# Kernel tuning notes

Measured on AMD Instinct MI355X. Metric: run time of the kernel, lower is better.

## Reference

```python
import jax, jax.numpy as jnp
import numpy as np

IMAGE_WEIGHT = 0.0736196319
EXAM_WEIGHTS = np.array([0.0736196319, 0.09202453988, 0.1042944785, 0.1042944785,
                         0.1877300613, 0.06257668712, 0.06257668712, 0.2346625767,
                         0.0782208589], dtype=np.float32)


def setup_inputs() -> dict:
    key = jax.random.key(0)
    k1, k2, k3 = jax.random.split(key, 3)
    B, L, C = 128, 8192, 10
    # probabilities / soft labels in (0,1); keep away from exact 0/1 so log() is finite
    pred = jax.random.uniform(k1, (B, L, C), dtype=jnp.float32) * 0.98 + 0.01
    label = jax.random.uniform(k2, (B, L, C), dtype=jnp.float32) * 0.98 + 0.01
    seq_lens = jax.random.randint(k3, (B,), 1, L + 1, dtype=jnp.int32)
    return {"pred": pred, "label": label, "seq_lens": seq_lens}


def reference(pred, label, seq_lens):
    B, L, C = pred.shape
    w = jnp.asarray(EXAM_WEIGHTS, dtype=pred.dtype)          # [9]
    lens = seq_lens.astype(pred.dtype)                        # [B]
    mask = (jnp.arange(L)[None, :] < seq_lens[:, None]).astype(pred.dtype)  # [B, L]

    # ---- exam-level loss: BCE between per-exam masked means, weighted per channel ----
    pm = jnp.einsum('blc,bl->bc', pred[..., 1:], mask) / lens[:, None]   # [B, 9]
    ym = jnp.einsum('blc,bl->bc', label[..., 1:], mask) / lens[:, None]  # [B, 9]
    exam_bce = -(ym * jnp.log(pm) + (1.0 - ym) * jnp.log(1.0 - pm))      # [B, 9]
    exam_loss = jnp.sum(exam_bce * w[None, :])
    total_weights = B * jnp.sum(w)

    # ---- image-level loss: per-element BCE weighted by image_weight * mean(label_0) ----
    p0 = pred[..., 0]   # [B, L]
    y0 = label[..., 0]  # [B, L]
    y0_mean = jnp.sum(y0 * mask, axis=1) / lens                          # [B]
    img_w = IMAGE_WEIGHT * y0_mean                                       # [B]
    img_bce = -(y0 * jnp.log(p0) + (1.0 - y0) * jnp.log(1.0 - p0)) * mask  # [B, L]
    image_loss = jnp.sum(jnp.sum(img_bce, axis=1) * img_w)
    total_weights = total_weights + jnp.sum(img_w * lens)

    return (exam_loss + image_loss) / total_weights
```

## Files before the change

### kernel.cpp

```cpp
#include <hip/hip_runtime.h>


#define L_DIM 8192
#define B_DIM 128
#define C_DIM 10
#define SPLIT 8

#define IMAGE_WEIGHT 0.0736196319f

__device__ __constant__ float EXAM_W[9] = {
    0.0736196319f, 0.09202453988f, 0.1042944785f, 0.1042944785f,
    0.1877300613f, 0.06257668712f, 0.06257668712f, 0.2346625767f,
    0.0782208589f};

__device__ __forceinline__ float bce0(float p, float y) {
  return -(y * __logf(p) + (1.0f - y) * __logf(1.0f - p));
}

__global__ __launch_bounds__(256) void rsna_partial_kernel(
    const float* __restrict__ pred, const float* __restrict__ label,
    const int* __restrict__ seq_lens, float* __restrict__ slots) {
  const int b = blockIdx.x;
  const int s = blockIdx.y;
  const int len = seq_lens[b];
  const int chunk = ((len + 2 * SPLIT - 1) / (2 * SPLIT)) * 2;
  const int start = s * chunk;
  const int end = min(start + chunk, len);

  float sp[9], sl[9];
#pragma unroll
  for (int c = 0; c < 9; ++c) {
    sp[c] = 0.0f;
    sl[c] = 0.0f;
  }
  float sy0 = 0.0f;
  float sbce = 0.0f;

  for (int l = start + 2 * (int)threadIdx.x; l < end; l += 512) {
    const size_t base = ((size_t)b * L_DIM + (size_t)l) * C_DIM;
    if (l + 1 < end) {
      const float4* p4 = reinterpret_cast<const float4*>(pred + base);
      const float4* y4 = reinterpret_cast<const float4*>(label + base);
      float p[20], y[20];
#pragma unroll
      for (int i = 0; i < 5; ++i) {
        float4 pv = p4[i];
        float4 yv = y4[i];
        p[4 * i] = pv.x; p[4 * i + 1] = pv.y; p[4 * i + 2] = pv.z; p[4 * i + 3] = pv.w;
        y[4 * i] = yv.x; y[4 * i + 1] = yv.y; y[4 * i + 2] = yv.z; y[4 * i + 3] = yv.w;
      }
#pragma unroll
      for (int c = 0; c < 9; ++c) {
        sp[c] += p[c + 1] + p[c + 11];
        sl[c] += y[c + 1] + y[c + 11];
      }
      sy0 += y[0] + y[10];
      sbce += bce0(p[0], y[0]) + bce0(p[10], y[10]);
    } else {
      const float2* p2 = reinterpret_cast<const float2*>(pred + base);
      const float2* y2 = reinterpret_cast<const float2*>(label + base);
      float p[10], y[10];
#pragma unroll
      for (int i = 0; i < 5; ++i) {
        float2 pv = p2[i];
        float2 yv = y2[i];
        p[2 * i] = pv.x; p[2 * i + 1] = pv.y;
        y[2 * i] = yv.x; y[2 * i + 1] = yv.y;
      }
#pragma unroll
      for (int c = 0; c < 9; ++c) {
        sp[c] += p[c + 1];
        sl[c] += y[c + 1];
      }
      sy0 += y[0];
      sbce += bce0(p[0], y[0]);
    }
  }

  float vals[20];
#pragma unroll
  for (int c = 0; c < 9; ++c) {
    vals[c] = sp[c];
    vals[9 + c] = sl[c];
  }
  vals[18] = sy0;
  vals[19] = sbce;

#pragma unroll
  for (int i = 0; i < 20; ++i) {
    float v = vals[i];
#pragma unroll
    for (int off = 32; off > 0; off >>= 1) v += __shfl_down(v, off, 64);
    vals[i] = v;
  }

  __shared__ float lds[4][20];
  const int wave = threadIdx.x >> 6;
  const int lane = threadIdx.x & 63;
  if (lane == 0) {
#pragma unroll
    for (int i = 0; i < 20; ++i) lds[wave][i] = vals[i];
  }
  __syncthreads();
  if (threadIdx.x < 20) {
    slots[(b * SPLIT + s) * 20 + (int)threadIdx.x] =
        lds[0][threadIdx.x] + lds[1][threadIdx.x] + lds[2][threadIdx.x] +
        lds[3][threadIdx.x];
  }
}

__global__ __launch_bounds__(128) void rsna_final_kernel(
    const float* __restrict__ slots, const int* __restrict__ seq_lens,
    float* __restrict__ out) {
  const int b = threadIdx.x;
  float r[20];
#pragma unroll
  for (int i = 0; i < 20; ++i) r[i] = 0.0f;
  const float* base = slots + b * SPLIT * 20;
#pragma unroll
  for (int s = 0; s < SPLIT; ++s)
#pragma unroll
    for (int i = 0; i < 20; ++i) r[i] += base[s * 20 + i];

  const float len = (float)seq_lens[b];
  const float inv_len = 1.0f / len;

  float exam = 0.0f;
#pragma unroll
  for (int c = 0; c < 9; ++c) {
    const float pm = r[c] * inv_len;
    const float ym = r[9 + c] * inv_len;
    exam += EXAM_W[c] * (-(ym * __logf(pm) + (1.0f - ym) * __logf(1.0f - pm)));
  }
  const float sy0 = r[18];
  const float sbce = r[19];
  const float img_w = IMAGE_WEIGHT * sy0 * inv_len;
  float numer = exam + sbce * img_w;
  float wext = IMAGE_WEIGHT * sy0;

#pragma unroll
  for (int off = 32; off > 0; off >>= 1) {
    numer += __shfl_down(numer, off, 64);
    wext += __shfl_down(wext, off, 64);
  }

  __shared__ float lds[4];
  if ((threadIdx.x & 63) == 0) {
    const int wave = threadIdx.x >> 6;
    lds[wave * 2] = numer;
    lds[wave * 2 + 1] = wext;
  }
  __syncthreads();
  if (threadIdx.x == 0) {
    float wsum = 0.0f;
#pragma unroll
    for (int c = 0; c < 9; ++c) wsum += EXAM_W[c];
    const float n = lds[0] + lds[2];
    const float w = lds[1] + lds[3];
    out[0] = n / ((float)B_DIM * wsum + w);
  }
}

extern "C" void kernel_launch(void* const* d_in, const int* in_sizes, int n_in,
                              void* d_out, int out_size, void* d_ws,
                              size_t ws_size, hipStream_t stream) {
  const float* pred = (const float*)d_in[0];
  const float* label = (const float*)d_in[1];
  const int* seq_lens = (const int*)d_in[2];
  float* slots = (float*)d_ws;

  dim3 grid(B_DIM, SPLIT);
  rsna_partial_kernel<<<grid, 256, 0, stream>>>(pred, label, seq_lens, slots);
  rsna_final_kernel<<<1, 128, 0, stream>>>(slots, seq_lens, (float*)d_out);
}
```

Before: 114.1 us.

## Fuse final reduction into partial kernel via atomics and last-block counters

```diff
diff --git a/kernel.cpp b/kernel.cpp
--- a/kernel.cpp
+++ b/kernel.cpp
@@ -8,6 +8,11 @@
 
 #define IMAGE_WEIGHT 0.0736196319f
 
+#define GNUM_IDX 2560
+#define GWEXT_IDX 2561
+#define ICTR_IDX 2562
+#define WS_ZERO_BYTES ((2562 + 129) * 4)
+
 __device__ __constant__ float EXAM_W[9] = {
     0.0736196319f, 0.09202453988f, 0.1042944785f, 0.1042944785f,
     0.1877300613f, 0.06257668712f, 0.06257668712f, 0.2346625767f,
@@ -17,9 +22,10 @@
   return -(y * __logf(p) + (1.0f - y) * __logf(1.0f - p));
 }
 
-__global__ __launch_bounds__(256) void rsna_partial_kernel(
+__global__ __launch_bounds__(256) void rsna_fused_kernel(
     const float* __restrict__ pred, const float* __restrict__ label,
-    const int* __restrict__ seq_lens, float* __restrict__ slots) {
+    const int* __restrict__ seq_lens, float* __restrict__ ws,
+    float* __restrict__ out) {
   const int b = blockIdx.x;
   const int s = blockIdx.y;
   const int len = seq_lens[b];
@@ -103,61 +109,54 @@
   }
   __syncthreads();
   if (threadIdx.x < 20) {
-    slots[(b * SPLIT + s) * 20 + (int)threadIdx.x] =
-        lds[0][threadIdx.x] + lds[1][threadIdx.x] + lds[2][threadIdx.x] +
-        lds[3][threadIdx.x];
-  }
-}
-
-__global__ __launch_bounds__(128) void rsna_final_kernel(
-    const float* __restrict__ slots, const int* __restrict__ seq_lens,
-    float* __restrict__ out) {
-  const int b = threadIdx.x;
-  float r[20];
-#pragma unroll
-  for (int i = 0; i < 20; ++i) r[i] = 0.0f;
-  const float* base = slots + b * SPLIT * 20;
-#pragma unroll
-  for (int s = 0; s < SPLIT; ++s)
-#pragma unroll
-    for (int i = 0; i < 20; ++i) r[i] += base[s * 20 + i];
-
-  const float len = (float)seq_lens[b];
-  const float inv_len = 1.0f / len;
-
-  float exam = 0.0f;
-#pragma unroll
-  for (int c = 0; c < 9; ++c) {
-    const float pm = r[c] * inv_len;
-    const float ym = r[9 + c] * inv_len;
-    exam += EXAM_W[c] * (-(ym * __logf(pm) + (1.0f - ym) * __logf(1.0f - pm)));
-  }
-  const float sy0 = r[18];
-  const float sbce = r[19];
-  const float img_w = IMAGE_WEIGHT * sy0 * inv_len;
-  float numer = exam + sbce * img_w;
-  float wext = IMAGE_WEIGHT * sy0;
-
-#pragma unroll
-  for (int off = 32; off > 0; off >>= 1) {
-    numer += __shfl_down(numer, off, 64);
-    wext += __shfl_down(wext, off, 64);
-  }
-
-  __shared__ float lds[4];
-  if ((threadIdx.x & 63) == 0) {
-    const int wave = threadIdx.x >> 6;
-    lds[wave * 2] = numer;
-    lds[wave * 2 + 1] = wext;
+    const float v = lds[0][threadIdx.x] + lds[1][threadIdx.x] +
+                    lds[2][threadIdx.x] + lds[3][threadIdx.x];
+    atomicAdd(&ws[b * 20 + (int)threadIdx.x], v);
   }
   __syncthreads();
-  if (threadIdx.x == 0) {
-    float wsum = 0.0f;
+
+  int* ictr = (int*)(ws + ICTR_IDX);
+
+  if (threadIdx.x < 64) {
+    int t = 0;
+    if (threadIdx.x == 0) {
+      __threadfence();
+      t = atomicAdd(&ictr[b], 1);
+    }
+    t = __shfl(t, 0, 64);
+    if (t == SPLIT - 1) {
+      float v = 0.0f;
+      if (threadIdx.x < 20) v = atomicAdd(&ws[b * 20 + (int)threadIdx.x], 0.0f);
+      float r[20];
 #pragma unroll
-    for (int c = 0; c < 9; ++c) wsum += EXAM_W[c];
-    const float n = lds[0] + lds[2];
-    const float w = lds[1] + lds[3];
-    out[0] = n / ((float)B_DIM * wsum + w);
+      for (int i = 0; i < 20; ++i) r[i] = __shfl(v, i, 64);
+      if (threadIdx.x == 0) {
+        const float inv_len = 1.0f / (float)len;
+        float exam = 0.0f;
+#pragma unroll
+        for (int c = 0; c < 9; ++c) {
+          const float pm = r[c] * inv_len;
+          const float ym = r[9 + c] * inv_len;
+          exam += EXAM_W[c] *
+                  (-(ym * __logf(pm) + (1.0f - ym) * __logf(1.0f - pm)));
+        }
+        const float img_w = IMAGE_WEIGHT * r[18] * inv_len;
+        const float numer = exam + r[19] * img_w;
+        const float wext = IMAGE_WEIGHT * r[18];
+        atomicAdd(&ws[GNUM_IDX], numer);
+        atomicAdd(&ws[GWEXT_IDX], wext);
+        __threadfence();
+        const int t2 = atomicAdd(&ictr[B_DIM], 1);
+        if (t2 == B_DIM - 1) {
+          const float n = atomicAdd(&ws[GNUM_IDX], 0.0f);
+          const float w = atomicAdd(&ws[GWEXT_IDX], 0.0f);
+          float wsum = 0.0f;
+#pragma unroll
+          for (int c = 0; c < 9; ++c) wsum += EXAM_W[c];
+          out[0] = n / ((float)B_DIM * wsum + w);
+        }
+      }
+    }
   }
 }
 
@@ -167,9 +166,10 @@
   const float* pred = (const float*)d_in[0];
   const float* label = (const float*)d_in[1];
   const int* seq_lens = (const int*)d_in[2];
-  float* slots = (float*)d_ws;
+  float* ws = (float*)d_ws;
 
+  hipMemsetAsync(d_ws, 0, WS_ZERO_BYTES, stream);
   dim3 grid(B_DIM, SPLIT);
-  rsna_partial_kernel<<<grid, 256, 0, stream>>>(pred, label, seq_lens, slots);
-  rsna_final_kernel<<<1, 128, 0, stream>>>(slots, seq_lens, (float*)d_out);
+  rsna_fused_kernel<<<grid, 256, 0, stream>>>(pred, label, seq_lens, ws,
+                                              (float*)d_out);
 }
```

Result: slower. 154.3 us (+35.2%).

## Double sequence split, drop the row loop, and reduce partials with atomics

Applied to the files above, without the earlier changes.

```diff
diff --git a/kernel.cpp b/kernel.cpp
--- a/kernel.cpp
+++ b/kernel.cpp
@@ -4,7 +4,7 @@
 #define L_DIM 8192
 #define B_DIM 128
 #define C_DIM 10
-#define SPLIT 8
+#define SPLIT 16
 
 #define IMAGE_WEIGHT 0.0736196319f
 
@@ -19,7 +19,7 @@
 
 __global__ __launch_bounds__(256) void rsna_partial_kernel(
     const float* __restrict__ pred, const float* __restrict__ label,
-    const int* __restrict__ seq_lens, float* __restrict__ slots) {
+    const int* __restrict__ seq_lens, float* __restrict__ row_acc) {
   const int b = blockIdx.x;
   const int s = blockIdx.y;
   const int len = seq_lens[b];
@@ -36,7 +36,8 @@
   float sy0 = 0.0f;
   float sbce = 0.0f;
 
-  for (int l = start + 2 * (int)threadIdx.x; l < end; l += 512) {
+  const int l = start + 2 * (int)threadIdx.x;
+  if (l < end) {
     const size_t base = ((size_t)b * L_DIM + (size_t)l) * C_DIM;
     if (l + 1 < end) {
       const float4* p4 = reinterpret_cast<const float4*>(pred + base);
@@ -51,11 +52,11 @@
       }
 #pragma unroll
       for (int c = 0; c < 9; ++c) {
-        sp[c] += p[c + 1] + p[c + 11];
-        sl[c] += y[c + 1] + y[c + 11];
+        sp[c] = p[c + 1] + p[c + 11];
+        sl[c] = y[c + 1] + y[c + 11];
       }
-      sy0 += y[0] + y[10];
-      sbce += bce0(p[0], y[0]) + bce0(p[10], y[10]);
+      sy0 = y[0] + y[10];
+      sbce = bce0(p[0], y[0]) + bce0(p[10], y[10]);
     } else {
       const float2* p2 = reinterpret_cast<const float2*>(pred + base);
       const float2* y2 = reinterpret_cast<const float2*>(label + base);
@@ -69,11 +70,11 @@
       }
 #pragma unroll
       for (int c = 0; c < 9; ++c) {
-        sp[c] += p[c + 1];
-        sl[c] += y[c + 1];
+        sp[c] = p[c + 1];
+        sl[c] = y[c + 1];
       }
-      sy0 += y[0];
-      sbce += bce0(p[0], y[0]);
+      sy0 = y[0];
+      sbce = bce0(p[0], y[0]);
     }
   }
 
@@ -103,25 +104,17 @@
   }
   __syncthreads();
   if (threadIdx.x < 20) {
-    slots[(b * SPLIT + s) * 20 + (int)threadIdx.x] =
-        lds[0][threadIdx.x] + lds[1][threadIdx.x] + lds[2][threadIdx.x] +
-        lds[3][threadIdx.x];
+    const float v = lds[0][threadIdx.x] + lds[1][threadIdx.x] +
+                    lds[2][threadIdx.x] + lds[3][threadIdx.x];
+    atomicAdd(&row_acc[b * 20 + (int)threadIdx.x], v);
   }
 }
 
 __global__ __launch_bounds__(128) void rsna_final_kernel(
-    const float* __restrict__ slots, const int* __restrict__ seq_lens,
+    const float* __restrict__ row_acc, const int* __restrict__ seq_lens,
     float* __restrict__ out) {
   const int b = threadIdx.x;
-  float r[20];
-#pragma unroll
-  for (int i = 0; i < 20; ++i) r[i] = 0.0f;
-  const float* base = slots + b * SPLIT * 20;
-#pragma unroll
-  for (int s = 0; s < SPLIT; ++s)
-#pragma unroll
-    for (int i = 0; i < 20; ++i) r[i] += base[s * 20 + i];
-
+  const float* r = row_acc + b * 20;
   const float len = (float)seq_lens[b];
   const float inv_len = 1.0f / len;
 
@@ -167,9 +160,10 @@
   const float* pred = (const float*)d_in[0];
   const float* label = (const float*)d_in[1];
   const int* seq_lens = (const int*)d_in[2];
-  float* slots = (float*)d_ws;
+  float* row_acc = (float*)d_ws;
 
+  hipMemsetAsync(d_ws, 0, B_DIM * 20 * sizeof(float), stream);
   dim3 grid(B_DIM, SPLIT);
-  rsna_partial_kernel<<<grid, 256, 0, stream>>>(pred, label, seq_lens, slots);
-  rsna_final_kernel<<<1, 128, 0, stream>>>(slots, seq_lens, (float*)d_out);
+  rsna_partial_kernel<<<grid, 256, 0, stream>>>(pred, label, seq_lens, row_acc);
+  rsna_final_kernel<<<1, 128, 0, stream>>>(row_acc, seq_lens, (float*)d_out);
 }
```

Measured after the change: 113.7 us. About the same (-0.3%).
